# Optimization experiments

Measured on AMD Instinct MI355X. Metric: run time of the kernel, lower is better.

## Reference

```python
import jax, jax.numpy as jnp
import numpy as np


def setup_inputs() -> dict:
    key = jax.random.key(0)
    k1, k2, k3 = jax.random.split(key, 3)
    B, C, K, H, W = 256, 2048, 18, 24, 8
    feat = jax.random.normal(k1, (B, C, H, W), dtype=jnp.float32)
    masks = jax.random.uniform(k2, (B, K, H, W), dtype=jnp.float32)
    pool_global_feat = jax.random.normal(k3, (B, C), dtype=jnp.float32)
    return {"feat": feat, "masks": masks, "pool_global_feat": pool_global_feat}


def reference(feat, masks, pool_global_feat):
    # For each landmark k: spatial mean of mask_k * feat  -> [B, C, K]
    # einsum reads feat once instead of 18 passes.
    B, C, H, W = feat.shape
    hw = jnp.asarray(H * W, feat.dtype)
    # [B, C, K] = sum_{hw} masks[b,k,h,w] * feat[b,c,h,w] / (H*W)
    pg = jnp.einsum('bkhw,bchw->bck', masks, feat) / hw
    # AdaptiveMaxPool1d(1) over the landmark axis -> [B, C]
    pg_max = jnp.max(pg, axis=2)
    # concat with global pooled feature -> [B, 2C]
    return jnp.concatenate([pool_global_feat, pg_max], axis=1)
```

## Files before the change

kernel.cpp:

```cpp
#include <hip/hip_runtime.h>

#define BB 256
#define CC 2048
#define KK 18
#define HWW 192
#define CH_PER_THREAD 4
#define BLOCK 256

__global__ __launch_bounds__(BLOCK, 2)
void pgfa_pose_guided_kernel(const float* __restrict__ feat,
                             const float* __restrict__ masks,
                             const float* __restrict__ pgf,
                             float* __restrict__ out) {
    __shared__ float sm[KK][HWW];

    const int tid = threadIdx.x;
    const int b   = blockIdx.y;

    {
        const float4* m4 = (const float4*)(masks + (size_t)b * KK * HWW);
        float4* s4 = (float4*)(&sm[0][0]);
        for (int i = tid; i < (KK * HWW) / 4; i += BLOCK) s4[i] = m4[i];
    }
    __syncthreads();

    const int c0 = blockIdx.x * (BLOCK * CH_PER_THREAD) + tid * CH_PER_THREAD;
    const float* frow = feat + ((size_t)b * CC + (size_t)c0) * HWW;

    float acc[KK][CH_PER_THREAD];
    #pragma unroll
    for (int k = 0; k < KK; ++k)
        #pragma unroll
        for (int j = 0; j < CH_PER_THREAD; ++j) acc[k][j] = 0.0f;

    #pragma unroll 2
    for (int hw4 = 0; hw4 < HWW / 4; ++hw4) {
        float4 f[CH_PER_THREAD];
        #pragma unroll
        for (int j = 0; j < CH_PER_THREAD; ++j)
            f[j] = ((const float4*)(frow + j * HWW))[hw4];

        #pragma unroll
        for (int k = 0; k < KK; ++k) {
            const float4 m = ((const float4*)(&sm[k][0]))[hw4];
            #pragma unroll
            for (int j = 0; j < CH_PER_THREAD; ++j) {
                acc[k][j] += m.x * f[j].x;
                acc[k][j] += m.y * f[j].y;
                acc[k][j] += m.z * f[j].z;
                acc[k][j] += m.w * f[j].w;
            }
        }
    }

    const float inv_hw = 1.0f / (float)HWW;
    float4 res;
    float r[CH_PER_THREAD];
    #pragma unroll
    for (int j = 0; j < CH_PER_THREAD; ++j) {
        float v = acc[0][j];
        #pragma unroll
        for (int k = 1; k < KK; ++k) v = fmaxf(v, acc[k][j]);
        r[j] = v * inv_hw;
    }
    res.x = r[0]; res.y = r[1]; res.z = r[2]; res.w = r[3];

    float* orow = out + (size_t)b * (2 * CC);
    const float4 pg4 = ((const float4*)(pgf + (size_t)b * CC))[c0 / 4];
    ((float4*)orow)[c0 / 4] = pg4;
    ((float4*)(orow + CC))[c0 / 4] = res;
}

extern "C" void kernel_launch(void* const* d_in, const int* in_sizes, int n_in,
                              void* d_out, int out_size, void* d_ws, size_t ws_size,
                              hipStream_t stream) {
    const float* feat  = (const float*)d_in[0];
    const float* masks = (const float*)d_in[1];
    const float* pgf   = (const float*)d_in[2];
    float* out = (float*)d_out;

    dim3 grid(CC / (BLOCK * CH_PER_THREAD), BB);
    pgfa_pose_guided_kernel<<<grid, BLOCK, 0, stream>>>(feat, masks, pgf, out);
}
```

Baseline: 602.9 us.

## Stage feat tile in LDS with coalesced loads and split HW across thread groups

Each block now takes 64 channels and loads their feature rows into padded shared memory with fully coalesced float4 loads. Previously each thread strided through its own channel rows, so global reads were uncoalesced. Four thread groups each reduce a quarter of the spatial axis, with masks read from global/L1 (identical addresses across the 64 threads in a group) instead of shared memory. Partial sums are combined through shared memory before the max over landmarks. The grid grows from 512 to 8192 blocks, at the cost of an extra reduction step and heavier LDS use per block.

```diff
diff --git a/kernel.cpp b/kernel.cpp
--- a/kernel.cpp
+++ b/kernel.cpp
@@ -4,71 +4,81 @@
 #define CC 2048
 #define KK 18
 #define HWW 192
-#define CH_PER_THREAD 4
-#define BLOCK 256
+#define CT 64
+#define QQ 4
+#define QLEN (HWW / QQ)
+#define PADROW 196
+#define BLOCK (CT * QQ)
 
-__global__ __launch_bounds__(BLOCK, 2)
+__global__ __launch_bounds__(BLOCK)
 void pgfa_pose_guided_kernel(const float* __restrict__ feat,
                              const float* __restrict__ masks,
                              const float* __restrict__ pgf,
                              float* __restrict__ out) {
-    __shared__ float sm[KK][HWW];
+    __shared__ __align__(16) float lds[CT * PADROW];
 
     const int tid = threadIdx.x;
     const int b   = blockIdx.y;
+    const int c0  = blockIdx.x * CT;
 
     {
-        const float4* m4 = (const float4*)(masks + (size_t)b * KK * HWW);
-        float4* s4 = (float4*)(&sm[0][0]);
-        for (int i = tid; i < (KK * HWW) / 4; i += BLOCK) s4[i] = m4[i];
+        const float4* g4 = (const float4*)(feat + ((size_t)b * CC + c0) * HWW);
+        float4 tmp[12];
+        #pragma unroll
+        for (int n = 0; n < 12; ++n)
+            tmp[n] = g4[tid + n * BLOCK];
+        #pragma unroll
+        for (int n = 0; n < 12; ++n) {
+            int i  = tid + n * BLOCK;
+            int c  = i / (HWW / 4);
+            int h4 = i % (HWW / 4);
+            *(float4*)(&lds[c * PADROW + h4 * 4]) = tmp[n];
+        }
     }
     __syncthreads();
 
-    const int c0 = blockIdx.x * (BLOCK * CH_PER_THREAD) + tid * CH_PER_THREAD;
-    const float* frow = feat + ((size_t)b * CC + (size_t)c0) * HWW;
+    const int c = tid & (CT - 1);
+    const int q = tid >> 6;
 
-    float acc[KK][CH_PER_THREAD];
+    const float* mq   = masks + (size_t)b * KK * HWW + q * QLEN;
+    const float* frow = &lds[c * PADROW + q * QLEN];
+
+    float acc[KK];
     #pragma unroll
-    for (int k = 0; k < KK; ++k)
-        #pragma unroll
-        for (int j = 0; j < CH_PER_THREAD; ++j) acc[k][j] = 0.0f;
+    for (int k = 0; k < KK; ++k) acc[k] = 0.0f;
 
     #pragma unroll 2
-    for (int hw4 = 0; hw4 < HWW / 4; ++hw4) {
-        float4 f[CH_PER_THREAD];
-        #pragma unroll
-        for (int j = 0; j < CH_PER_THREAD; ++j)
-            f[j] = ((const float4*)(frow + j * HWW))[hw4];
-
+    for (int j = 0; j < QLEN / 4; ++j) {
+        const float4 f = *(const float4*)(frow + j * 4);
         #pragma unroll
         for (int k = 0; k < KK; ++k) {
-            const float4 m = ((const float4*)(&sm[k][0]))[hw4];
-            #pragma unroll
-            for (int j = 0; j < CH_PER_THREAD; ++j) {
-                acc[k][j] += m.x * f[j].x;
-                acc[k][j] += m.y * f[j].y;
-                acc[k][j] += m.z * f[j].z;
-                acc[k][j] += m.w * f[j].w;
-            }
+            const float4 m = *(const float4*)(mq + k * HWW + j * 4);
+            acc[k] += m.x * f.x;
+            acc[k] += m.y * f.y;
+            acc[k] += m.z * f.z;
+            acc[k] += m.w * f.w;
         }
     }
 
-    const float inv_hw = 1.0f / (float)HWW;
-    float4 res;
-    float r[CH_PER_THREAD];
+    __syncthreads();
+    float* part = lds;
     #pragma unroll
-    for (int j = 0; j < CH_PER_THREAD; ++j) {
-        float v = acc[0][j];
+    for (int k = 0; k < KK; ++k)
+        part[c * (KK * QQ) + k * QQ + q] = acc[k];
+    __syncthreads();
+
+    if (tid < CT) {
+        float vmax = -INFINITY;
         #pragma unroll
-        for (int k = 1; k < KK; ++k) v = fmaxf(v, acc[k][j]);
-        r[j] = v * inv_hw;
+        for (int k = 0; k < KK; ++k) {
+            const float4 p = *(const float4*)(&part[tid * (KK * QQ) + k * QQ]);
+            const float s = (p.x + p.y) + (p.z + p.w);
+            vmax = fmaxf(vmax, s);
+        }
+        float* orow = out + (size_t)b * (2 * CC);
+        orow[c0 + tid]      = pgf[(size_t)b * CC + c0 + tid];
+        orow[CC + c0 + tid] = vmax * (1.0f / (float)HWW);
     }
-    res.x = r[0]; res.y = r[1]; res.z = r[2]; res.w = r[3];
-
-    float* orow = out + (size_t)b * (2 * CC);
-    const float4 pg4 = ((const float4*)(pgf + (size_t)b * CC))[c0 / 4];
-    ((float4*)orow)[c0 / 4] = pg4;
-    ((float4*)(orow + CC))[c0 / 4] = res;
 }
 
 extern "C" void kernel_launch(void* const* d_in, const int* in_sizes, int n_in,
@@ -79,6 +89,6 @@
     const float* pgf   = (const float*)d_in[2];
     float* out = (float*)d_out;
 
-    dim3 grid(CC / (BLOCK * CH_PER_THREAD), BB);
+    dim3 grid(CC / CT, BB);
     pgfa_pose_guided_kernel<<<grid, BLOCK, 0, stream>>>(feat, masks, pgf, out);
 }
```

Measured after the change: 680.8 us. +12.9%, slower.
